# Performance work log

Measured on AMD Instinct MI355X. Metric: run time of the kernel, lower is better.

## Reference

```python
import jax, jax.numpy as jnp
import numpy as np

B, N, DIM = 8, 1024, 1024
HEADS, DIM_HEAD = 16, 64
INNER = HEADS * DIM_HEAD  # 1024


def setup_inputs() -> dict:
    key = jax.random.key(0)
    k1, k2, k3 = jax.random.split(key, 3)
    x = jax.random.normal(k1, (B, N, DIM), dtype=jnp.float32)
    # Dense kernels (Glorot-ish scale for numerical sanity)
    w_qkv = jax.random.normal(k2, (DIM, 3 * INNER), dtype=jnp.float32) * (DIM ** -0.5)
    w_out = jax.random.normal(k3, (INNER, DIM), dtype=jnp.float32) * (INNER ** -0.5)
    b_out = jnp.zeros((DIM,), dtype=jnp.float32)
    return {"x": x, "w_qkv": w_qkv, "w_out": w_out, "b_out": b_out}


def reference(x, w_qkv, w_out, b_out):
    scale = DIM_HEAD ** -0.5
    qkv = x @ w_qkv                                   # [B, N, 3*INNER]
    q, k, v = jnp.split(qkv, 3, axis=-1)              # each [B, N, INNER]

    def to_heads(t):
        # [B, N, H*Dh] -> [B, H, N, Dh]
        return t.reshape(B, N, HEADS, DIM_HEAD).transpose(0, 2, 1, 3)

    q, k, v = to_heads(q), to_heads(k), to_heads(v)
    dots = jnp.einsum("bhid,bhjd->bhij", q, k) * scale   # [B, H, N, N]
    attn = jax.nn.softmax(dots, axis=-1)
    out = jnp.einsum("bhij,bhjd->bhid", attn, v)          # [B, H, N, Dh]
    out = out.transpose(0, 2, 1, 3).reshape(B, N, INNER)  # merge heads
    return out @ w_out + b_out                            # project_out (dropout inactive at inference)
```

## Files before the change

### kernel.cpp

```cpp
#include <hip/hip_runtime.h>
#include <hip/hip_bf16.h>
#include <math.h>

typedef __bf16 bf16_t;
typedef __bf16 bf16x2 __attribute__((ext_vector_type(2)));
typedef __bf16 bf16x4 __attribute__((ext_vector_type(4)));
typedef __bf16 bf16x8 __attribute__((ext_vector_type(8)));
typedef float f32x4 __attribute__((ext_vector_type(4)));
typedef float f32x16 __attribute__((ext_vector_type(16)));

#define LOG2E 1.44269504088896340736f

#define GL2LDS(g, l)                                                     \
  __builtin_amdgcn_global_load_lds(                                      \
      (const __attribute__((address_space(1))) unsigned int*)(g),        \
      (__attribute__((address_space(3))) unsigned int*)(l), 16, 0, 0)

#define BAR() asm volatile("s_barrier" ::: "memory")
#define VMCNT(n) asm volatile("s_waitcnt vmcnt(" #n ")" ::: "memory")
#define LGKM0()                                         \
  do {                                                  \
    asm volatile("s_waitcnt lgkmcnt(0)" ::: "memory");  \
    __builtin_amdgcn_sched_barrier(0);                  \
  } while (0)

static __device__ __forceinline__ unsigned pk2(bf16_t a, bf16_t b) {
  bf16x2 t;
  t[0] = a;
  t[1] = b;
  return __builtin_bit_cast(unsigned, t);
}

__global__ __launch_bounds__(256) void convert_f32_bf16(const float* __restrict__ in,
                                                        bf16_t* __restrict__ out) {
  const size_t idx = (size_t)(blockIdx.x * 256 + threadIdx.x) * 8;
  f32x4 a = *(const f32x4*)&in[idx];
  f32x4 b = *(const f32x4*)&in[idx + 4];
  bf16x8 v;
#pragma unroll
  for (int i = 0; i < 4; i++) { v[i] = (bf16_t)a[i]; v[i + 4] = (bf16_t)b[i]; }
  *(bf16x8*)&out[idx] = v;
}

__global__ __launch_bounds__(256) void transpose_f32_bf16(const float* __restrict__ in,
                                                          bf16_t* __restrict__ out,
                                                          int R, int C) {
  __shared__ bf16_t t[64][65];
  const int c0 = blockIdx.x * 64, r0 = blockIdx.y * 64;
  const int tx = threadIdx.x, ty = threadIdx.y;
#pragma unroll
  for (int i = 0; i < 16; i++) {
    int r = ty + i * 4;
    t[r][tx] = (bf16_t)in[(size_t)(r0 + r) * C + c0 + tx];
  }
  __syncthreads();
#pragma unroll
  for (int i = 0; i < 16; i++) {
    int r = ty + i * 4;
    out[(size_t)(c0 + r) * R + r0 + tx] = t[tx][r];
  }
}

template <int MODE, int NW>
__global__ __launch_bounds__(256, 4) void gemmT(const bf16_t* __restrict__ A,
                                                const bf16_t* __restrict__ Bt,
                                                bf16_t* __restrict__ Qb,
                                                bf16_t* __restrict__ Kb,
                                                bf16_t* __restrict__ Vtb,
                                                const float* __restrict__ bias,
                                                float* __restrict__ Out) {
  constexpr int K = 1024;
  constexpr int NT = K / 32;
  constexpr int BN = NW * 32;
  __shared__ __align__(16) bf16_t As[3][128 * 32];
  __shared__ __align__(16) bf16_t Bs[3][BN * 32];
  const int gx = gridDim.x;
  const int lin = blockIdx.y * gx + blockIdx.x;
  const int per = (gx * gridDim.y) >> 3;
  const int swz = (lin & 7) * per + (lin >> 3);
  const int m0 = (swz / gx) * 128, n0 = (swz % gx) * BN;
  const int tid = threadIdx.x;
  const int w = tid >> 6, l = tid & 63;
  const int lr = l & 15, lq = l >> 4;
  const int wm = w >> 1, wn = w & 1;

  const int rs = tid >> 2, ps = tid & 3;
  const int cs = (ps ^ ((rs >> 1) & 3)) * 8;
  const size_t gA0 = (size_t)(m0 + rs) * K + cs;
  const size_t gA1 = (size_t)(m0 + 64 + rs) * K + cs;
  const size_t gB0 = (size_t)(n0 + rs) * K + cs;
  const size_t gB1 = (size_t)(n0 + 64 + rs) * K + cs;
  const int ldsu0 = (w * 64) * 8;
  const int ldsu1 = (256 + w * 64) * 8;

#define STG(bf_, kt_)                                          \
  do {                                                         \
    const size_t kk_ = (size_t)(kt_) * 32;                     \
    GL2LDS(&A[gA0 + kk_], &As[bf_][ldsu0]);                    \
    GL2LDS(&A[gA1 + kk_], &As[bf_][ldsu1]);                    \
    GL2LDS(&Bt[gB0 + kk_], &Bs[bf_][ldsu0]);                   \
    if constexpr (NW == 4) GL2LDS(&Bt[gB1 + kk_], &Bs[bf_][ldsu1]); \
  } while (0)

  int aoff[4], boff[NW];
#pragma unroll
  for (int mf = 0; mf < 4; mf++) {
    const int row = wm * 64 + mf * 16 + lr;
    aoff[mf] = row * 32 + ((lq ^ ((row >> 1) & 3)) << 3);
  }
#pragma unroll
  for (int nf = 0; nf < NW; nf++) {
    const int row = wn * (NW * 16) + nf * 16 + lr;
    boff[nf] = row * 32 + ((lq ^ ((row >> 1) & 3)) << 3);
  }

  f32x4 acc[4][NW] = {};

  STG(0, 0);
  STG(1, 1);
  if constexpr (NW == 4) { VMCNT(4); } else { VMCNT(3); }
  BAR();

  for (int t = 0; t < NT; ++t) {
    const int bufR = t % 3;
    if (t + 2 < NT) STG((t + 2) % 3, t + 2);
    bf16x8 af[4], bv[NW];
#pragma unroll
    for (int mf = 0; mf < 4; mf++)
      af[mf] = *(const bf16x8*)&As[bufR][aoff[mf]];
#pragma unroll
    for (int nf = 0; nf < NW; nf++)
      bv[nf] = *(const bf16x8*)&Bs[bufR][boff[nf]];
    LGKM0();
    __builtin_amdgcn_s_setprio(1);
#pragma unroll
    for (int mf = 0; mf < 4; mf++)
#pragma unroll
      for (int nf = 0; nf < NW; nf++)
        acc[mf][nf] = __builtin_amdgcn_mfma_f32_16x16x32_bf16(af[mf], bv[nf],
                                                              acc[mf][nf], 0, 0, 0);
    __builtin_amdgcn_s_setprio(0);
    if (t == NT - 2) {
      VMCNT(0);
    } else if (t < NT - 2) {
      if constexpr (NW == 4) { VMCNT(4); } else { VMCNT(3); }
    }
    BAR();
  }

#pragma unroll
  for (int mf = 0; mf < 4; mf++)
#pragma unroll
    for (int nf = 0; nf < NW; nf++)
#pragma unroll
      for (int i = 0; i < 4; i++) {
        const int m = m0 + wm * 64 + mf * 16 + lq * 4 + i;
        const int c = n0 + wn * (NW * 16) + nf * 16 + lr;
        const float v = acc[mf][nf][i];
        if (MODE == 1) {
          Out[(size_t)m * 1024 + c] = v + bias[c];
        } else {
          const int b = m >> 10, n = m & 1023;
          const int which = c >> 10, cc = c & 1023;
          const int hh = cc >> 6, d = cc & 63;
          const size_t qk = ((size_t)((b * 16 + hh) * 1024 + n)) * 64 + d;
          if (which == 0)
            Qb[qk] = (bf16_t)(v * (0.125f * LOG2E));
          else if (which == 1)
            Kb[qk] = (bf16_t)v;
          else
            Vtb[((size_t)((b * 16 + hh) * 64 + d)) * 1024 + n] = (bf16_t)v;
        }
      }
}

__global__ __launch_bounds__(256) void attn128(const bf16_t* __restrict__ Qb,
                                               const bf16_t* __restrict__ Kb,
                                               const bf16_t* __restrict__ Vtb,
                                               bf16_t* __restrict__ Ob) {
  __shared__ __align__(16) bf16_t Ks[2][64 * 64];
  __shared__ __align__(16) bf16_t Vs[2][64 * 64];
  const int bid = blockIdx.x;
  const int qt = bid >> 7, b = (bid >> 4) & 7, h = bid & 15;
  const bf16_t* Qh = Qb + (size_t)((b * 16 + h) * 1024) * 64;
  const bf16_t* Kh = Kb + (size_t)((b * 16 + h) * 1024) * 64;
  const bf16_t* Vh = Vtb + (size_t)((b * 16 + h) * 64) * 1024;
  const int tid = threadIdx.x, w = tid >> 6, l = tid & 63;
  const int lq31 = l & 31, hi = l >> 5;
  const int q0w = qt * 128 + w * 32;
  const int ksw = lq31 & 7;

  const int r0 = tid >> 3, p0 = tid & 7;
  const int ck = (p0 ^ (r0 & 7)) * 8;
  const int ldsS0 = (w * 64) * 8;
  const int ldsS1 = (256 + w * 64) * 8;

#define STGKV(bf_, j_)                                                  \
  do {                                                                  \
    const size_t jb = (size_t)(j_) * 64;                                \
    GL2LDS(&Kh[(jb + r0) * 64 + ck], &Ks[bf_][ldsS0]);                  \
    GL2LDS(&Kh[(jb + r0 + 32) * 64 + ck], &Ks[bf_][ldsS1]);             \
    GL2LDS(&Vh[(size_t)r0 * 1024 + jb + ck], &Vs[bf_][ldsS0]);          \
    GL2LDS(&Vh[(size_t)(r0 + 32) * 1024 + jb + ck], &Vs[bf_][ldsS1]);   \
  } while (0)

  bf16x8 qf[4];
#pragma unroll
  for (int c = 0; c < 4; c++)
    qf[c] = *(const bf16x8*)&Qh[(size_t)(q0w + lq31) * 64 + c * 16 + hi * 8];

  STGKV(0, 0);
  VMCNT(0);
  BAR();

  f32x16 o0 = {}, o1 = {};
  float denom = 0.0f;

  for (int it = 0; it < 16; ++it) {
    const int buf = it & 1;
    if (it < 15) STGKV(buf ^ 1, it + 1);
    f32x16 s0 = {}, s1 = {};
    __builtin_amdgcn_s_setprio(1);
#pragma unroll
    for (int c = 0; c < 4; c++) {
      const int col = ((c * 2 + hi) ^ ksw) << 3;
      bf16x8 kf0 = *(const bf16x8*)&Ks[buf][lq31 * 64 + col];
      bf16x8 kf1 = *(const bf16x8*)&Ks[buf][(32 + lq31) * 64 + col];
      s0 = __builtin_amdgcn_mfma_f32_32x32x16_bf16(kf0, qf[c], s0, 0, 0, 0);
      s1 = __builtin_amdgcn_mfma_f32_32x32x16_bf16(kf1, qf[c], s1, 0, 0, 0);
    }
    __builtin_amdgcn_s_setprio(0);
    unsigned wds[16];
    float dl = 0.0f;
#pragma unroll
    for (int j = 0; j < 8; j++) {
      bf16_t e0 = (bf16_t)exp2f(s0[2 * j]), e1 = (bf16_t)exp2f(s0[2 * j + 1]);
      dl += (float)e0 + (float)e1;
      wds[j] = pk2(e0, e1);
    }
#pragma unroll
    for (int j = 0; j < 8; j++) {
      bf16_t e0 = (bf16_t)exp2f(s1[2 * j]), e1 = (bf16_t)exp2f(s1[2 * j + 1]);
      dl += (float)e0 + (float)e1;
      wds[8 + j] = pk2(e0, e1);
    }
    denom += dl + __shfl_xor(dl, 32);
    bf16x8 pf[4];
#pragma unroll
    for (int q2 = 0; q2 < 4; q2++) {
      const int base = (q2 >> 1) * 8 + (q2 & 1) * 4;
      const unsigned a0 = wds[base], a1 = wds[base + 1];
      const unsigned a2 = wds[base + 2], a3 = wds[base + 3];
      const unsigned x0 = __shfl_xor(a0, 32), x1 = __shfl_xor(a1, 32);
      const unsigned x2 = __shfl_xor(a2, 32), x3 = __shfl_xor(a3, 32);
      union { unsigned u[4]; bf16x8 v; } u;
      u.u[0] = hi ? x2 : a0;
      u.u[1] = hi ? x3 : a1;
      u.u[2] = hi ? a2 : x0;
      u.u[3] = hi ? a3 : x1;
      pf[q2] = u.v;
    }
    __builtin_amdgcn_s_setprio(1);
#pragma unroll
    for (int c = 0; c < 4; c++) {
      const int col = ((c * 2 + hi) ^ ksw) << 3;
      bf16x8 vf0 = *(const bf16x8*)&Vs[buf][lq31 * 64 + col];
      bf16x8 vf1 = *(const bf16x8*)&Vs[buf][(32 + lq31) * 64 + col];
      o0 = __builtin_amdgcn_mfma_f32_32x32x16_bf16(vf0, pf[c], o0, 0, 0, 0);
      o1 = __builtin_amdgcn_mfma_f32_32x32x16_bf16(vf1, pf[c], o1, 0, 0, 0);
    }
    __builtin_amdgcn_s_setprio(0);
    VMCNT(0);
    BAR();
  }
  const float inv = 1.0f / denom;
  const int grow = b * 1024 + q0w + lq31;
#pragma unroll
  for (int db = 0; db < 2; db++)
#pragma unroll
    for (int rg = 0; rg < 4; rg++) {
      bf16x4 ov;
#pragma unroll
      for (int i = 0; i < 4; i++)
        ov[i] = (bf16_t)((db ? o1[rg * 4 + i] : o0[rg * 4 + i]) * inv);
      *(bf16x4*)&Ob[(size_t)grow * 1024 + h * 64 + db * 32 + rg * 8 + hi * 4] = ov;
    }
}

extern "C" void kernel_launch(void* const* d_in, const int* in_sizes, int n_in,
                              void* d_out, int out_size, void* d_ws, size_t ws_size,
                              hipStream_t stream) {
  const float* x     = (const float*)d_in[0];
  const float* w_qkv = (const float*)d_in[1];
  const float* w_out = (const float*)d_in[2];
  const float* b_out = (const float*)d_in[3];
  float* out = (float*)d_out;

  bf16_t* ws = (bf16_t*)d_ws;
  const size_t SZ = (size_t)8 * 1024 * 1024;
  bf16_t* Qb  = ws;
  bf16_t* Kb  = Qb + SZ;
  bf16_t* Vtb = Kb + SZ;
  bf16_t* Ob  = Vtb + SZ;
  bf16_t* Wqt = Ob + SZ;
  bf16_t* Wot = Wqt + (size_t)3072 * 1024;
  bf16_t* Xb  = Ob;

  hipLaunchKernelGGL(convert_f32_bf16, dim3(4096), dim3(256), 0, stream, x, Xb);
  hipLaunchKernelGGL(transpose_f32_bf16, dim3(48, 16), dim3(64, 4), 0, stream,
                     w_qkv, Wqt, 1024, 3072);
  hipLaunchKernelGGL(transpose_f32_bf16, dim3(16, 16), dim3(64, 4), 0, stream,
                     w_out, Wot, 1024, 1024);
  hipLaunchKernelGGL((gemmT<0, 4>), dim3(24, 64), dim3(256), 0, stream,
                     Xb, Wqt, Qb, Kb, Vtb, (const float*)nullptr, (float*)nullptr);
  hipLaunchKernelGGL(attn128, dim3(1024), dim3(256), 0, stream, Qb, Kb, Vtb, Ob);
  hipLaunchKernelGGL((gemmT<1, 2>), dim3(16, 64), dim3(256), 0, stream,
                     Ob, Wot, (bf16_t*)nullptr, (bf16_t*)nullptr, (bf16_t*)nullptr,
                     b_out, out);
}
```

Before: 282.2 us.

## Load K and V fragments directly from global memory instead of LDS staging

```diff
diff --git a/kernel.cpp b/kernel.cpp
--- a/kernel.cpp
+++ b/kernel.cpp
@@ -178,8 +178,6 @@
                                                const bf16_t* __restrict__ Kb,
                                                const bf16_t* __restrict__ Vtb,
                                                bf16_t* __restrict__ Ob) {
-  __shared__ __align__(16) bf16_t Ks[2][64 * 64];
-  __shared__ __align__(16) bf16_t Vs[2][64 * 64];
   const int bid = blockIdx.x;
   const int qt = bid >> 7, b = (bid >> 4) & 7, h = bid & 15;
   const bf16_t* Qh = Qb + (size_t)((b * 16 + h) * 1024) * 64;
@@ -188,48 +186,42 @@
   const int tid = threadIdx.x, w = tid >> 6, l = tid & 63;
   const int lq31 = l & 31, hi = l >> 5;
   const int q0w = qt * 128 + w * 32;
-  const int ksw = lq31 & 7;
-
-  const int r0 = tid >> 3, p0 = tid & 7;
-  const int ck = (p0 ^ (r0 & 7)) * 8;
-  const int ldsS0 = (w * 64) * 8;
-  const int ldsS1 = (256 + w * 64) * 8;
-
-#define STGKV(bf_, j_)                                                  \
-  do {                                                                  \
-    const size_t jb = (size_t)(j_) * 64;                                \
-    GL2LDS(&Kh[(jb + r0) * 64 + ck], &Ks[bf_][ldsS0]);                  \
-    GL2LDS(&Kh[(jb + r0 + 32) * 64 + ck], &Ks[bf_][ldsS1]);             \
-    GL2LDS(&Vh[(size_t)r0 * 1024 + jb + ck], &Vs[bf_][ldsS0]);          \
-    GL2LDS(&Vh[(size_t)(r0 + 32) * 1024 + jb + ck], &Vs[bf_][ldsS1]);   \
-  } while (0)
 
   bf16x8 qf[4];
 #pragma unroll
   for (int c = 0; c < 4; c++)
     qf[c] = *(const bf16x8*)&Qh[(size_t)(q0w + lq31) * 64 + c * 16 + hi * 8];
 
-  STGKV(0, 0);
-  VMCNT(0);
-  BAR();
+  const bf16_t* kb0 = &Kh[(size_t)lq31 * 64 + hi * 8];
+  const bf16_t* kb1 = &Kh[(size_t)(32 + lq31) * 64 + hi * 8];
+  const bf16_t* vb0 = &Vh[(size_t)lq31 * 1024 + hi * 8];
+  const bf16_t* vb1 = &Vh[(size_t)(32 + lq31) * 1024 + hi * 8];
 
   f32x16 o0 = {}, o1 = {};
   float denom = 0.0f;
 
   for (int it = 0; it < 16; ++it) {
-    const int buf = it & 1;
-    if (it < 15) STGKV(buf ^ 1, it + 1);
+    const int jb = it * 64;
+    bf16x8 kf0[4], kf1[4];
+#pragma unroll
+    for (int c = 0; c < 4; c++) {
+      kf0[c] = *(const bf16x8*)&kb0[(size_t)jb * 64 + c * 16];
+      kf1[c] = *(const bf16x8*)&kb1[(size_t)jb * 64 + c * 16];
+    }
     f32x16 s0 = {}, s1 = {};
     __builtin_amdgcn_s_setprio(1);
 #pragma unroll
     for (int c = 0; c < 4; c++) {
-      const int col = ((c * 2 + hi) ^ ksw) << 3;
-      bf16x8 kf0 = *(const bf16x8*)&Ks[buf][lq31 * 64 + col];
-      bf16x8 kf1 = *(const bf16x8*)&Ks[buf][(32 + lq31) * 64 + col];
-      s0 = __builtin_amdgcn_mfma_f32_32x32x16_bf16(kf0, qf[c], s0, 0, 0, 0);
-      s1 = __builtin_amdgcn_mfma_f32_32x32x16_bf16(kf1, qf[c], s1, 0, 0, 0);
+      s0 = __builtin_amdgcn_mfma_f32_32x32x16_bf16(kf0[c], qf[c], s0, 0, 0, 0);
+      s1 = __builtin_amdgcn_mfma_f32_32x32x16_bf16(kf1[c], qf[c], s1, 0, 0, 0);
     }
     __builtin_amdgcn_s_setprio(0);
+    bf16x8 vf0[4], vf1[4];
+#pragma unroll
+    for (int c = 0; c < 4; c++) {
+      vf0[c] = *(const bf16x8*)&vb0[jb + c * 16];
+      vf1[c] = *(const bf16x8*)&vb1[jb + c * 16];
+    }
     unsigned wds[16];
     float dl = 0.0f;
 #pragma unroll
@@ -263,15 +255,10 @@
     __builtin_amdgcn_s_setprio(1);
 #pragma unroll
     for (int c = 0; c < 4; c++) {
-      const int col = ((c * 2 + hi) ^ ksw) << 3;
-      bf16x8 vf0 = *(const bf16x8*)&Vs[buf][lq31 * 64 + col];
-      bf16x8 vf1 = *(const bf16x8*)&Vs[buf][(32 + lq31) * 64 + col];
-      o0 = __builtin_amdgcn_mfma_f32_32x32x16_bf16(vf0, pf[c], o0, 0, 0, 0);
-      o1 = __builtin_amdgcn_mfma_f32_32x32x16_bf16(vf1, pf[c], o1, 0, 0, 0);
+      o0 = __builtin_amdgcn_mfma_f32_32x32x16_bf16(vf0[c], pf[c], o0, 0, 0, 0);
+      o1 = __builtin_amdgcn_mfma_f32_32x32x16_bf16(vf1[c], pf[c], o1, 0, 0, 0);
     }
     __builtin_amdgcn_s_setprio(0);
-    VMCNT(0);
-    BAR();
   }
   const float inv = 1.0f / denom;
   const int grow = b * 1024 + q0w + lq31;
```

Result: slower. 357.1 us (+26.6%).
